# Optimization experiments

Measured on AMD Instinct MI355X. Metric: run time of the kernel, lower is better.

Reference implementation:

```python
import jax, jax.numpy as jnp
import numpy as np
from jax import lax

# IVF+PQ search (FAISS IVF1024,PQ8x8 with nprobe=32, by_residual=False variant):
# 1) coarse quantizer: L2 distance of each query to nlist centroids, keep top nprobe lists
# 2) ADC: per-query LUT of squared distances between query subvectors and PQ codebooks,
#    database distance = sum over subquantizers of LUT gathered at the stored codes
# 3) mask database vectors whose IVF list was not probed, return indices of top_k smallest

NPROBE = 32  # top_n_centroids
BIG = jnp.float32(1e30)


def setup_inputs() -> dict:
    key = jax.random.key(0)
    ks = jax.random.split(key, 5)
    Q, D = 256, 128
    M, K = 8, 256          # pq_subvecs, 2**pq_nbits
    dsub = D // M          # 16
    nlist = 1024
    N = 250_000            # database size
    queries = jax.random.normal(ks[0], (Q, D), dtype=jnp.float32)
    centroids = jax.random.normal(ks[1], (nlist, D), dtype=jnp.float32)
    codebooks = jax.random.normal(ks[2], (M, K, dsub), dtype=jnp.float32)
    db_codes = jax.random.randint(ks[3], (N, M), 0, K, dtype=jnp.int32)
    db_list = jax.random.randint(ks[4], (N,), 0, nlist, dtype=jnp.int32)
    return {"queries": queries, "centroids": centroids, "codebooks": codebooks,
            "db_codes": db_codes, "db_list": db_list, "top_k": 100}


def _masked_adc_distances(queries, centroids, codebooks, db_codes, db_list):
    Q, D = queries.shape
    nlist = centroids.shape[0]
    M, K, dsub = codebooks.shape
    # ---- coarse quantizer: ||q - c||^2 over [Q, nlist] ----
    coarse = (jnp.sum(queries * queries, -1, keepdims=True)
              + jnp.sum(centroids * centroids, -1)[None, :]
              - 2.0 * queries @ centroids.T)
    _, probed = lax.top_k(-coarse, NPROBE)                      # [Q, NPROBE] list ids
    probe_mask = jnp.zeros((Q, nlist), dtype=bool).at[
        jnp.arange(Q)[:, None], probed].set(True)               # [Q, nlist]
    allowed = probe_mask[:, db_list]                            # [Q, N]
    # ---- PQ ADC lookup table: ||q_sub - codeword||^2, [Q, M, K] ----
    qs = queries.reshape(Q, M, dsub)
    lut = (jnp.sum(qs * qs, -1)[:, :, None]
           + jnp.sum(codebooks * codebooks, -1)[None, :, :]
           - 2.0 * jnp.einsum('qmd,mkd->qmk', qs, codebooks))   # [Q, M, K]
    # ---- accumulate gathered LUT entries over subquantizers ----
    dist = lut[:, 0, db_codes[:, 0]]                            # [Q, N]
    for m in range(1, M):
        dist = dist + lut[:, m, db_codes[:, m]]
    return jnp.where(allowed, dist, BIG)


def reference(queries, centroids, codebooks, db_codes, db_list, top_k):
    dist = _masked_adc_distances(queries, centroids, codebooks, db_codes, db_list)
    _, indices = lax.top_k(-dist, top_k)                        # smallest distances
    return indices
```

## Files before the change

kernel.cpp:

```cpp
#include <hip/hip_runtime.h>

#define DDIM 128
#define MSUB 8
#define KCODE 256
#define DSUB 16
#define NLIST 1024
#define NPROBE 32
#define TOPK 100
#define HBINS 4096
#define COLL_CAP 2048
#define RCAP 12
#define SCHUNK 1024


__device__ __forceinline__ float xla_sumsq128(const float* x) {
  float s[16];
  #pragma unroll
  for (int j = 0; j < 16; ++j) {
    float p0 = __fmul_rn(x[j],       x[j]);
    float p1 = __fmul_rn(x[j + 16],  x[j + 16]);
    float p2 = __fmul_rn(x[j + 32],  x[j + 32]);
    float p3 = __fmul_rn(x[j + 48],  x[j + 48]);
    float p4 = __fmul_rn(x[j + 64],  x[j + 64]);
    float p5 = __fmul_rn(x[j + 80],  x[j + 80]);
    float p6 = __fmul_rn(x[j + 96],  x[j + 96]);
    float p7 = __fmul_rn(x[j + 112], x[j + 112]);
    float r0 = __fadd_rn(p0, p4);
    float r1 = __fadd_rn(p1, p5);
    float r2 = __fadd_rn(p2, p6);
    float r3 = __fadd_rn(p3, p7);
    s[j] = __fadd_rn(__fadd_rn(r0, r1), __fadd_rn(r2, r3));
  }
  float a[8], b[4], c[2];
  #pragma unroll
  for (int j = 0; j < 8; ++j) a[j] = __fadd_rn(s[j], s[j + 8]);
  #pragma unroll
  for (int j = 0; j < 4; ++j) b[j] = __fadd_rn(a[j], a[j + 4]);
  #pragma unroll
  for (int j = 0; j < 2; ++j) c[j] = __fadd_rn(b[j], b[j + 2]);
  return __fadd_rn(c[0], c[1]);
}

__device__ __forceinline__ float xla_sumsq16(const float* x) {
  float p[16];
  #pragma unroll
  for (int j = 0; j < 16; ++j) p[j] = __fmul_rn(x[j], x[j]);
  float s8[8], s4[4], s2[2];
  #pragma unroll
  for (int j = 0; j < 8; ++j) s8[j] = __fadd_rn(p[j], p[j + 8]);
  #pragma unroll
  for (int j = 0; j < 4; ++j) s4[j] = __fadd_rn(s8[j], s8[j + 4]);
  #pragma unroll
  for (int j = 0; j < 2; ++j) s2[j] = __fadd_rn(s4[j], s4[j + 2]);
  return __fadd_rn(s2[0], s2[1]);
}

__device__ __forceinline__ float chain_dot16(const float* a, const float* b) {
  float dot = 0.f;
  #pragma unroll
  for (int d = 0; d < DSUB; ++d) dot = __fmaf_rn(a[d], b[d], dot);
  return dot;
}

__device__ __forceinline__ float adc_dist(const float* lut, unsigned long long code) {
  float d = lut[(unsigned)(code & 255ULL)];
  d = __fadd_rn(d, lut[256  + (unsigned)((code >> 8)  & 255ULL)]);
  d = __fadd_rn(d, lut[512  + (unsigned)((code >> 16) & 255ULL)]);
  d = __fadd_rn(d, lut[768  + (unsigned)((code >> 24) & 255ULL)]);
  d = __fadd_rn(d, lut[1024 + (unsigned)((code >> 32) & 255ULL)]);
  d = __fadd_rn(d, lut[1280 + (unsigned)((code >> 40) & 255ULL)]);
  d = __fadd_rn(d, lut[1536 + (unsigned)((code >> 48) & 255ULL)]);
  d = __fadd_rn(d, lut[1792 + (unsigned)((code >> 56) & 255ULL)]);
  return d;
}

__device__ __forceinline__ unsigned block_scan_incl(unsigned v, volatile unsigned* wsum,
                                                    int t, int nwaves) {
  int lane = t & 63, wid = t >> 6;
  #pragma unroll
  for (int off = 1; off < 64; off <<= 1) {
    unsigned u = __shfl_up(v, off, 64);
    if (lane >= off) v += u;
  }
  if (lane == 63) wsum[wid] = v;
  __syncthreads();
  if (wid == 0 && lane < nwaves) {
    unsigned wv = wsum[lane];
    #pragma unroll
    for (int off = 1; off < 16; off <<= 1) {
      unsigned u = __shfl_up(wv, off, 64);
      if (lane >= off) wv += u;
    }
    wsum[lane] = wv;
  }
  __syncthreads();
  return v + (wid > 0 ? wsum[wid - 1] : 0u);
}

__global__ __launch_bounds__(256) void k_coarse_lut(const float* __restrict__ queries,
                                                    const float* __restrict__ centroids,
                                                    const float* __restrict__ codebooks,
                                                    const int* __restrict__ db_list, int N,
                                                    float* __restrict__ lut_g,
                                                    int* __restrict__ probed,
                                                    unsigned* __restrict__ counts) {
  const int qi = blockIdx.x;
  const int t = threadIdx.x;
  __shared__ float qs[DDIM];
  __shared__ unsigned hist[HBINS];
  __shared__ unsigned long long coll[512];
  __shared__ unsigned wsum[4];
  __shared__ unsigned scnt;
  __shared__ int sT32;
  if (t < DDIM) qs[t] = queries[qi * DDIM + t];
  for (int i = t; i < HBINS; i += 256) hist[i] = 0;
  if (t == 0) { scnt = 0; sT32 = HBINS - 1; }
  __syncthreads();

  for (int j = 0; j < MSUB; ++j) {
    int idx = j * KCODE + t;
    const float* cb = codebooks + (size_t)idx * DSUB;
    const float* qsub = qs + j * DSUB;
    float cbv[DSUB], qv[DSUB];
    #pragma unroll
    for (int d = 0; d < DSUB; ++d) { cbv[d] = cb[d]; qv[d] = qsub[d]; }
    const float qq16 = xla_sumsq16(qv);
    const float cc16 = xla_sumsq16(cbv);
    const float dot16 = chain_dot16(qv, cbv);
    lut_g[(size_t)qi * (MSUB * KCODE) + idx] =
        __fsub_rn(__fadd_rn(qq16, cc16), __fmul_rn(2.0f, dot16));
  }

  const float qq = xla_sumsq128(qs);
  unsigned long long keys[4];
  #pragma unroll
  for (int w = 0; w < 4; ++w) {
    int c = t + 256 * w;
    const float* cr = centroids + (size_t)c * DDIM;
    float cbuf[DDIM];
    #pragma unroll
    for (int d = 0; d < DDIM; d += 4) {
      float4 cv = *(const float4*)(cr + d);
      cbuf[d] = cv.x; cbuf[d + 1] = cv.y; cbuf[d + 2] = cv.z; cbuf[d + 3] = cv.w;
    }
    const float cc = xla_sumsq128(cbuf);
    float dot = 0.f;
    #pragma unroll
    for (int d = 0; d < DDIM; ++d) dot = __fmaf_rn(qs[d], cbuf[d], dot);
    float dist = __fsub_rn(__fadd_rn(qq, cc), __fmul_rn(2.0f, dot));
    unsigned bits = __float_as_uint(dist);
    keys[w] = ((unsigned long long)bits << 32) | (unsigned)c;
    atomicAdd(&hist[bits >> 19], 1u);
  }
  __syncthreads();

  unsigned mysum = 0;
  #pragma unroll
  for (int i = 0; i < 16; ++i) mysum += hist[t * 16 + i];
  unsigned incl = block_scan_incl(mysum, wsum, t, 4);
  unsigned excl = incl - mysum;
  if (excl < NPROBE && NPROBE <= incl) {
    unsigned c2 = excl;
    for (int i = 0; i < 16; ++i) {
      unsigned h = hist[t * 16 + i];
      if (c2 + h >= NPROBE) { sT32 = t * 16 + i; break; }
      c2 += h;
    }
  }
  __syncthreads();
  const int T32 = sT32;
  #pragma unroll
  for (int w = 0; w < 4; ++w) {
    if ((int)(keys[w] >> 51) <= T32) {
      unsigned p = atomicAdd(&scnt, 1u);
      if (p < 512) coll[p] = keys[w];
    }
  }
  __syncthreads();
  unsigned cnt = scnt; if (cnt > 512) cnt = 512;
  for (unsigned i = t; i < cnt; i += 256) {
    unsigned long long key = coll[i];
    unsigned r = 0;
    for (unsigned j = 0; j < cnt; ++j) r += (coll[j] < key) ? 1u : 0u;
    if (r < NPROBE) probed[qi * NPROBE + r] = (int)(key & 0xffffffffULL);
  }
  __syncthreads();

  for (int i = t; i < NLIST; i += 256) hist[i] = 0;
  __syncthreads();
  for (int n = qi * 256 + t; n < N; n += 256 * 256)
    atomicAdd(&hist[db_list[n]], 1u);
  __syncthreads();
  for (int i = t; i < NLIST; i += 256)
    if (hist[i]) atomicAdd(&counts[i], hist[i]);
}

__global__ __launch_bounds__(1024) void k_scan(const unsigned* __restrict__ counts,
                                               unsigned* __restrict__ bstart) {
  __shared__ unsigned s[NLIST];
  const int t = threadIdx.x;
  unsigned mine = counts[t];
  s[t] = mine;
  __syncthreads();
  for (int off = 1; off < NLIST; off <<= 1) {
    unsigned v = (t >= off) ? s[t - off] : 0u;
    __syncthreads();
    s[t] += v;
    __syncthreads();
  }
  bstart[t + 1] = s[t];
  if (t == 0) bstart[0] = 0;
}

__global__ __launch_bounds__(256) void k_scatter(const int* __restrict__ db_list,
                                                 const int* __restrict__ db_codes, int N,
                                                 const unsigned* __restrict__ bstart,
                                                 unsigned* __restrict__ cursor,
                                                 int4* __restrict__ pack) {
  __shared__ unsigned lhist[NLIST], lbase[NLIST];
  const int t = threadIdx.x;
  const int base = blockIdx.x * SCHUNK;
  for (int i = t; i < NLIST; i += 256) lhist[i] = 0;
  __syncthreads();
  #pragma unroll
  for (int k = 0; k < SCHUNK / 256; ++k) {
    int n = base + k * 256 + t;
    if (n < N) atomicAdd(&lhist[db_list[n]], 1u);
  }
  __syncthreads();
  for (int i = t; i < NLIST; i += 256) {
    unsigned cnt = lhist[i];
    if (cnt) lbase[i] = bstart[i] + atomicAdd(&cursor[i], cnt);
    lhist[i] = 0;
  }
  __syncthreads();
  #pragma unroll
  for (int k = 0; k < SCHUNK / 256; ++k) {
    int n = base + k * 256 + t;
    if (n < N) {
      int l = db_list[n];
      unsigned pos = lbase[l] + atomicAdd(&lhist[l], 1u);
      const int4* cp = (const int4*)(db_codes + (size_t)n * MSUB);
      int4 c0 = cp[0], c1 = cp[1];
      unsigned lo = (unsigned)(c0.x & 255) | ((unsigned)(c0.y & 255) << 8) |
                    ((unsigned)(c0.z & 255) << 16) | ((unsigned)(c0.w & 255) << 24);
      unsigned hi = (unsigned)(c1.x & 255) | ((unsigned)(c1.y & 255) << 8) |
                    ((unsigned)(c1.z & 255) << 16) | ((unsigned)(c1.w & 255) << 24);
      pack[pos] = make_int4((int)lo, (int)hi, n, 0);
    }
  }
}

__global__ __launch_bounds__(1024, 1) void k_search(const float* __restrict__ lut_g,
                                                    const int* __restrict__ probed,
                                                    const unsigned* __restrict__ bstart,
                                                    const int4* __restrict__ pack,
                                                    int* __restrict__ out) {
  const int qi = blockIdx.x;
  const int t = threadIdx.x;
  __shared__ float lut_s[MSUB * KCODE];
  __shared__ unsigned hist[HBINS];
  __shared__ unsigned long long coll[COLL_CAP];
  __shared__ unsigned pstart[NPROBE], pcum[NPROBE + 1];
  __shared__ unsigned wsum[16];
  __shared__ unsigned scnt;
  __shared__ int sT;

  for (int i = t; i < MSUB * KCODE; i += 1024) lut_s[i] = lut_g[(size_t)qi * (MSUB * KCODE) + i];
  if (t < NPROBE) {
    int l = probed[qi * NPROBE + t];
    unsigned s0 = bstart[l];
    pstart[t] = s0;
    pcum[t + 1] = bstart[l + 1] - s0;
  }
  for (int i = t; i < HBINS; i += 1024) hist[i] = 0;
  if (t == 0) { scnt = 0; sT = HBINS - 1; }
  __syncthreads();
  if (t == 0) {
    unsigned acc = 0;
    pcum[0] = 0;
    for (int j = 1; j <= NPROBE; ++j) { acc += pcum[j]; pcum[j] = acc; }
  }
  __syncthreads();
  const unsigned total = pcum[NPROBE];

  unsigned regbits[RCAP];
  {
    int s = 0;
    for (unsigned g = t; g < total; g += 1024, ++s) {
      int lo = 0, hi = NPROBE;
      while (hi - lo > 1) { int mid = (lo + hi) >> 1; if (pcum[mid] <= g) lo = mid; else hi = mid; }
      unsigned addr = pstart[lo] + (g - pcum[lo]);
      int4 w = pack[addr];
      unsigned long long code = (unsigned)w.x | ((unsigned long long)(unsigned)w.y << 32);
      unsigned bits = __float_as_uint(adc_dist(lut_s, code));
      if (s < RCAP) regbits[s] = bits;
      atomicAdd(&hist[bits >> 19], 1u);
    }
  }
  __syncthreads();

  {
    unsigned mysum = 0;
    #pragma unroll
    for (int i = 0; i < 4; ++i) mysum += hist[t * 4 + i];
    unsigned incl = block_scan_incl(mysum, wsum, t, 16);
    unsigned excl = incl - mysum;
    if (excl < TOPK && TOPK <= incl) {
      unsigned c = excl;
      #pragma unroll
      for (int i = 0; i < 4; ++i) {
        unsigned h = hist[t * 4 + i];
        if (c + h >= TOPK) { sT = t * 4 + i; break; }
        c += h;
      }
    }
  }
  __syncthreads();
  const int T = sT;

  {
    int s = 0;
    for (unsigned g = t; g < total; g += 1024, ++s) {
      unsigned bits;
      int lo = -1;
      if (s < RCAP) bits = regbits[s];
      else {
        int l2 = 0, hi = NPROBE;
        while (hi - l2 > 1) { int mid = (l2 + hi) >> 1; if (pcum[mid] <= g) l2 = mid; else hi = mid; }
        lo = l2;
        int4 w = pack[pstart[lo] + (g - pcum[lo])];
        unsigned long long code = (unsigned)w.x | ((unsigned long long)(unsigned)w.y << 32);
        bits = __float_as_uint(adc_dist(lut_s, code));
      }
      if ((int)(bits >> 19) <= T) {
        if (lo < 0) {
          int l2 = 0, hi = NPROBE;
          while (hi - l2 > 1) { int mid = (l2 + hi) >> 1; if (pcum[mid] <= g) l2 = mid; else hi = mid; }
          lo = l2;
        }
        unsigned n = (unsigned)pack[pstart[lo] + (g - pcum[lo])].z;
        unsigned p = atomicAdd(&scnt, 1u);
        if (p < COLL_CAP) coll[p] = ((unsigned long long)bits << 32) | n;
      }
    }
  }
  __syncthreads();

  unsigned cnt = scnt;
  if (cnt > COLL_CAP) cnt = COLL_CAP;
  for (unsigned i = t; i < cnt; i += 1024) {
    unsigned long long key = coll[i];
    unsigned r = 0;
    for (unsigned j = 0; j < cnt; ++j) r += (coll[j] < key) ? 1u : 0u;
    if (r < TOPK) out[qi * TOPK + r] = (int)(key & 0xffffffffULL);
  }
}

extern "C" void kernel_launch(void* const* d_in, const int* in_sizes, int n_in,
                              void* d_out, int out_size, void* d_ws, size_t ws_size,
                              hipStream_t stream) {
  const float* queries   = (const float*)d_in[0];
  const float* centroids = (const float*)d_in[1];
  const float* codebooks = (const float*)d_in[2];
  const int*   db_codes  = (const int*)d_in[3];
  const int*   db_list   = (const int*)d_in[4];
  const int N = in_sizes[4];
  const int Q = in_sizes[0] / DDIM;
  int* out = (int*)d_out;

  char* p = (char*)d_ws;
  float* lut_g = (float*)p;        p += (size_t)Q * MSUB * KCODE * 4;
  int* probed_g = (int*)p;         p += (size_t)Q * NPROBE * 4;
  unsigned* counts = (unsigned*)p; p += NLIST * 4;
  unsigned* cursor = (unsigned*)p; p += NLIST * 4;
  unsigned* bstart = (unsigned*)p; p += (NLIST + 4) * 4;
  int4* pack = (int4*)p;           p += (size_t)N * 16;

  hipMemsetAsync(counts, 0, (size_t)NLIST * 4 * 2, stream);

  k_coarse_lut<<<Q, 256, 0, stream>>>(queries, centroids, codebooks, db_list, N,
                                      lut_g, probed_g, counts);
  k_scan<<<1, 1024, 0, stream>>>(counts, bstart);
  k_scatter<<<(N + SCHUNK - 1) / SCHUNK, 256, 0, stream>>>(db_list, db_codes, N,
                                                           bstart, cursor, pack);
  k_search<<<Q, 1024, 0, stream>>>(lut_g, probed_g, bstart, pack, out);
}
```

Baseline: 135.6 us.

## Drop scan kernel, recompute list offsets in consumers, widen coarse kernel

Removes the single-block k_scan launch. k_scatter and k_search now each recompute the list-start prefix sum from the counts array in shared memory. k_coarse_lut is widened from 256 to 512 threads per block, with the LUT, centroid and histogram loops redistributed to match. k_search also keeps candidate addresses in registers so the second pass does not redo the binary search, and RCAP drops to 10 to offset the extra registers. The trade-off is redundant per-block scan work in exchange for one fewer launch and less dependent work inside the search.

```diff
diff --git a/kernel.cpp b/kernel.cpp
--- a/kernel.cpp
+++ b/kernel.cpp
@@ -9,7 +9,7 @@
 #define TOPK 100
 #define HBINS 4096
 #define COLL_CAP 2048
-#define RCAP 12
+#define RCAP 10
 #define SCHUNK 1024
 
 
@@ -97,7 +97,7 @@
   return v + (wid > 0 ? wsum[wid - 1] : 0u);
 }
 
-__global__ __launch_bounds__(256) void k_coarse_lut(const float* __restrict__ queries,
+__global__ __launch_bounds__(512) void k_coarse_lut(const float* __restrict__ queries,
                                                     const float* __restrict__ centroids,
                                                     const float* __restrict__ codebooks,
                                                     const int* __restrict__ db_list, int N,
@@ -109,16 +109,19 @@
   __shared__ float qs[DDIM];
   __shared__ unsigned hist[HBINS];
   __shared__ unsigned long long coll[512];
-  __shared__ unsigned wsum[4];
+  __shared__ unsigned wsum[16];
   __shared__ unsigned scnt;
   __shared__ int sT32;
   if (t < DDIM) qs[t] = queries[qi * DDIM + t];
-  for (int i = t; i < HBINS; i += 256) hist[i] = 0;
+  for (int i = t; i < HBINS; i += 512) hist[i] = 0;
   if (t == 0) { scnt = 0; sT32 = HBINS - 1; }
   __syncthreads();
 
-  for (int j = 0; j < MSUB; ++j) {
-    int idx = j * KCODE + t;
+  #pragma unroll
+  for (int jj = 0; jj < 4; ++jj) {
+    int j = jj * 2 + (t >> 8);
+    int k = t & 255;
+    int idx = j * KCODE + k;
     const float* cb = codebooks + (size_t)idx * DSUB;
     const float* qsub = qs + j * DSUB;
     float cbv[DSUB], qv[DSUB];
@@ -132,10 +135,10 @@
   }
 
   const float qq = xla_sumsq128(qs);
-  unsigned long long keys[4];
-  #pragma unroll
-  for (int w = 0; w < 4; ++w) {
-    int c = t + 256 * w;
+  unsigned long long keys[2];
+  #pragma unroll
+  for (int w = 0; w < 2; ++w) {
+    int c = t + 512 * w;
     const float* cr = centroids + (size_t)c * DDIM;
     float cbuf[DDIM];
     #pragma unroll
@@ -156,21 +159,22 @@
 
   unsigned mysum = 0;
   #pragma unroll
-  for (int i = 0; i < 16; ++i) mysum += hist[t * 16 + i];
-  unsigned incl = block_scan_incl(mysum, wsum, t, 4);
+  for (int i = 0; i < 8; ++i) mysum += hist[t * 8 + i];
+  unsigned incl = block_scan_incl(mysum, wsum, t, 8);
   unsigned excl = incl - mysum;
   if (excl < NPROBE && NPROBE <= incl) {
     unsigned c2 = excl;
-    for (int i = 0; i < 16; ++i) {
-      unsigned h = hist[t * 16 + i];
-      if (c2 + h >= NPROBE) { sT32 = t * 16 + i; break; }
+    #pragma unroll
+    for (int i = 0; i < 8; ++i) {
+      unsigned h = hist[t * 8 + i];
+      if (c2 + h >= NPROBE) { sT32 = t * 8 + i; break; }
       c2 += h;
     }
   }
   __syncthreads();
   const int T32 = sT32;
   #pragma unroll
-  for (int w = 0; w < 4; ++w) {
+  for (int w = 0; w < 2; ++w) {
     if ((int)(keys[w] >> 51) <= T32) {
       unsigned p = atomicAdd(&scnt, 1u);
       if (p < 512) coll[p] = keys[w];
@@ -178,7 +182,7 @@
   }
   __syncthreads();
   unsigned cnt = scnt; if (cnt > 512) cnt = 512;
-  for (unsigned i = t; i < cnt; i += 256) {
+  for (unsigned i = t; i < cnt; i += 512) {
     unsigned long long key = coll[i];
     unsigned r = 0;
     for (unsigned j = 0; j < cnt; ++j) r += (coll[j] < key) ? 1u : 0u;
@@ -186,40 +190,35 @@
   }
   __syncthreads();
 
-  for (int i = t; i < NLIST; i += 256) hist[i] = 0;
-  __syncthreads();
-  for (int n = qi * 256 + t; n < N; n += 256 * 256)
+  for (int i = t; i < NLIST; i += 512) hist[i] = 0;
+  __syncthreads();
+  for (int n = qi * 512 + t; n < N; n += 256 * 512)
     atomicAdd(&hist[db_list[n]], 1u);
   __syncthreads();
-  for (int i = t; i < NLIST; i += 256)
+  for (int i = t; i < NLIST; i += 512)
     if (hist[i]) atomicAdd(&counts[i], hist[i]);
-}
-
-__global__ __launch_bounds__(1024) void k_scan(const unsigned* __restrict__ counts,
-                                               unsigned* __restrict__ bstart) {
-  __shared__ unsigned s[NLIST];
-  const int t = threadIdx.x;
-  unsigned mine = counts[t];
-  s[t] = mine;
-  __syncthreads();
-  for (int off = 1; off < NLIST; off <<= 1) {
-    unsigned v = (t >= off) ? s[t - off] : 0u;
-    __syncthreads();
-    s[t] += v;
-    __syncthreads();
-  }
-  bstart[t + 1] = s[t];
-  if (t == 0) bstart[0] = 0;
 }
 
 __global__ __launch_bounds__(256) void k_scatter(const int* __restrict__ db_list,
                                                  const int* __restrict__ db_codes, int N,
-                                                 const unsigned* __restrict__ bstart,
+                                                 const unsigned* __restrict__ counts,
                                                  unsigned* __restrict__ cursor,
                                                  int4* __restrict__ pack) {
-  __shared__ unsigned lhist[NLIST], lbase[NLIST];
+  __shared__ unsigned lhist[NLIST], lbase[NLIST], sbstart[NLIST];
+  __shared__ unsigned wsum[16];
   const int t = threadIdx.x;
   const int base = blockIdx.x * SCHUNK;
+  {
+    unsigned c0 = counts[t * 4], c1 = counts[t * 4 + 1],
+             c2 = counts[t * 4 + 2], c3 = counts[t * 4 + 3];
+    unsigned sum4 = c0 + c1 + c2 + c3;
+    unsigned incl = block_scan_incl(sum4, wsum, t, 4);
+    unsigned excl = incl - sum4;
+    sbstart[t * 4] = excl;
+    sbstart[t * 4 + 1] = excl + c0;
+    sbstart[t * 4 + 2] = excl + c0 + c1;
+    sbstart[t * 4 + 3] = excl + c0 + c1 + c2;
+  }
   for (int i = t; i < NLIST; i += 256) lhist[i] = 0;
   __syncthreads();
   #pragma unroll
@@ -230,7 +229,7 @@
   __syncthreads();
   for (int i = t; i < NLIST; i += 256) {
     unsigned cnt = lhist[i];
-    if (cnt) lbase[i] = bstart[i] + atomicAdd(&cursor[i], cnt);
+    if (cnt) lbase[i] = sbstart[i] + atomicAdd(&cursor[i], cnt);
     lhist[i] = 0;
   }
   __syncthreads();
@@ -253,7 +252,7 @@
 
 __global__ __launch_bounds__(1024, 1) void k_search(const float* __restrict__ lut_g,
                                                     const int* __restrict__ probed,
-                                                    const unsigned* __restrict__ bstart,
+                                                    const unsigned* __restrict__ counts,
                                                     const int4* __restrict__ pack,
                                                     int* __restrict__ out) {
   const int qi = blockIdx.x;
@@ -261,20 +260,27 @@
   __shared__ float lut_s[MSUB * KCODE];
   __shared__ unsigned hist[HBINS];
   __shared__ unsigned long long coll[COLL_CAP];
+  __shared__ unsigned bst[NLIST + 1];
   __shared__ unsigned pstart[NPROBE], pcum[NPROBE + 1];
   __shared__ unsigned wsum[16];
   __shared__ unsigned scnt;
   __shared__ int sT;
 
   for (int i = t; i < MSUB * KCODE; i += 1024) lut_s[i] = lut_g[(size_t)qi * (MSUB * KCODE) + i];
+  {
+    unsigned v = counts[t];
+    unsigned incl = block_scan_incl(v, wsum, t, 16);
+    bst[t + 1] = incl;
+    if (t == 0) bst[0] = 0;
+  }
+  for (int i = t; i < HBINS; i += 1024) hist[i] = 0;
+  if (t == 0) { scnt = 0; sT = HBINS - 1; }
+  __syncthreads();
   if (t < NPROBE) {
     int l = probed[qi * NPROBE + t];
-    unsigned s0 = bstart[l];
-    pstart[t] = s0;
-    pcum[t + 1] = bstart[l + 1] - s0;
-  }
-  for (int i = t; i < HBINS; i += 1024) hist[i] = 0;
-  if (t == 0) { scnt = 0; sT = HBINS - 1; }
+    pstart[t] = bst[l];
+    pcum[t + 1] = bst[l + 1] - bst[l];
+  }
   __syncthreads();
   if (t == 0) {
     unsigned acc = 0;
@@ -284,7 +290,7 @@
   __syncthreads();
   const unsigned total = pcum[NPROBE];
 
-  unsigned regbits[RCAP];
+  unsigned regbits[RCAP], regaddr[RCAP];
   {
     int s = 0;
     for (unsigned g = t; g < total; g += 1024, ++s) {
@@ -294,7 +300,7 @@
       int4 w = pack[addr];
       unsigned long long code = (unsigned)w.x | ((unsigned long long)(unsigned)w.y << 32);
       unsigned bits = __float_as_uint(adc_dist(lut_s, code));
-      if (s < RCAP) regbits[s] = bits;
+      if (s < RCAP) { regbits[s] = bits; regaddr[s] = addr; }
       atomicAdd(&hist[bits >> 19], 1u);
     }
   }
@@ -322,24 +328,18 @@
   {
     int s = 0;
     for (unsigned g = t; g < total; g += 1024, ++s) {
-      unsigned bits;
-      int lo = -1;
-      if (s < RCAP) bits = regbits[s];
+      unsigned bits, addr;
+      if (s < RCAP) { bits = regbits[s]; addr = regaddr[s]; }
       else {
         int l2 = 0, hi = NPROBE;
         while (hi - l2 > 1) { int mid = (l2 + hi) >> 1; if (pcum[mid] <= g) l2 = mid; else hi = mid; }
-        lo = l2;
-        int4 w = pack[pstart[lo] + (g - pcum[lo])];
+        addr = pstart[l2] + (g - pcum[l2]);
+        int4 w = pack[addr];
         unsigned long long code = (unsigned)w.x | ((unsigned long long)(unsigned)w.y << 32);
         bits = __float_as_uint(adc_dist(lut_s, code));
       }
       if ((int)(bits >> 19) <= T) {
-        if (lo < 0) {
-          int l2 = 0, hi = NPROBE;
-          while (hi - l2 > 1) { int mid = (l2 + hi) >> 1; if (pcum[mid] <= g) l2 = mid; else hi = mid; }
-          lo = l2;
-        }
-        unsigned n = (unsigned)pack[pstart[lo] + (g - pcum[lo])].z;
+        unsigned n = (unsigned)pack[addr].z;
         unsigned p = atomicAdd(&scnt, 1u);
         if (p < COLL_CAP) coll[p] = ((unsigned long long)bits << 32) | n;
       }
@@ -374,15 +374,13 @@
   int* probed_g = (int*)p;         p += (size_t)Q * NPROBE * 4;
   unsigned* counts = (unsigned*)p; p += NLIST * 4;
   unsigned* cursor = (unsigned*)p; p += NLIST * 4;
-  unsigned* bstart = (unsigned*)p; p += (NLIST + 4) * 4;
   int4* pack = (int4*)p;           p += (size_t)N * 16;
 
   hipMemsetAsync(counts, 0, (size_t)NLIST * 4 * 2, stream);
 
-  k_coarse_lut<<<Q, 256, 0, stream>>>(queries, centroids, codebooks, db_list, N,
+  k_coarse_lut<<<Q, 512, 0, stream>>>(queries, centroids, codebooks, db_list, N,
                                       lut_g, probed_g, counts);
-  k_scan<<<1, 1024, 0, stream>>>(counts, bstart);
   k_scatter<<<(N + SCHUNK - 1) / SCHUNK, 256, 0, stream>>>(db_list, db_codes, N,
-                                                           bstart, cursor, pack);
-  k_search<<<Q, 1024, 0, stream>>>(lut_g, probed_g, bstart, pack, out);
-}
+                                                           counts, cursor, pack);
+  k_search<<<Q, 1024, 0, stream>>>(lut_g, probed_g, counts, pack, out);
+}
```

Result: slower. 172.6 us (+27.3%).
